# Optimization experiments

Hardware: AMD Instinct MI355X
Metric: run time of the kernel (lower is better)

## Reference

```python
import jax, jax.numpy as jnp
import numpy as np

H, W, L = 512, 512, 28
N_ITER = 12
SIGMA = 0.5
LAM = 1.0
PI = 3.141592653589793


def _offsets(s, phi_deg):
    # Matches torch: dx = s*cos(phi), dy = s*sin(phi), shifted to min 0, round-half-even.
    phi = phi_deg * PI / 180.0
    dx = s * np.cos(phi)
    dy = s * np.sin(phi)
    dx = dx - dx.min()
    dy = dy - dy.min()
    return np.rint(dx).astype(np.int32), np.rint(dy).astype(np.int32)


def _gauss_kernel(sigma):
    ksize = max(3, int(6 * sigma + 1) | 1)  # 5 for sigma=0.5
    ax = np.arange(ksize, dtype=np.float32) - ksize // 2
    g1 = np.exp(-0.5 * (ax / sigma) ** 2)
    g1 = g1 / g1.sum()
    g2 = np.outer(g1, g1).astype(np.float32)
    return jnp.asarray(g2)[None, None], ksize // 2  # [1,1,k,k], pad


def setup_inputs():
    k1, k2 = jax.random.split(jax.random.key(0))
    s_nom = jnp.arange(L, dtype=jnp.float32)
    phi_d_deg = jnp.ones((), dtype=jnp.float32)
    dx, dy = _offsets(np.arange(L, dtype=np.float32), 1.0)
    Hp, Wp = H + int(dy.max()), W + int(dx.max())
    y_1hw = jax.random.uniform(k1, (1, Hp, Wp), dtype=jnp.float32)
    mask2d = jax.random.uniform(k2, (H, W), dtype=jnp.float32)
    return {"y_1hw": y_1hw, "mask2d": mask2d, "phi_d_deg": phi_d_deg, "s_nom": s_nom}


def reference(y_1hw, mask2d, phi_d_deg, s_nom):
    # Integer dispersion offsets are detached (.item()) in the original, so they
    # are compile-time constants here.
    dx, dy = _offsets(np.asarray(s_nom), float(np.asarray(phi_d_deg)))
    Hp, Wp = H + int(dy.max()), W + int(dx.max())
    rows = dy[:, None, None] + np.arange(H, dtype=np.int64)[None, :, None]  # [L,H,1]
    cols = dx[:, None, None] + np.arange(W, dtype=np.int64)[None, None, :]  # [L,1,W]
    flat = jnp.asarray(rows * Wp + cols)  # [L,H,W] flat indices into [Hp*Wp]

    g2, pad = _gauss_kernel(SIGMA)

    def A(x):  # CASSI forward: [L,H,W] -> [Hp,Wp] batched scatter-add
        return jnp.zeros(Hp * Wp, x.dtype).at[flat].add(mask2d[None] * x).reshape(Hp, Wp)

    def At(y2):  # CASSI adjoint: [Hp,Wp] -> [L,H,W] batched gather
        return y2.reshape(-1)[flat] * mask2d[None]

    def denoise(x):  # depthwise 5x5 Gaussian; same 2D kernel per band -> bands as batch
        return jax.lax.conv_general_dilated(
            x[:, None], g2, (1, 1), [(pad, pad), (pad, pad)])[:, 0]

    # Phi_sum = sum over bands of shifted mask, clamped to >= 1
    Phi_sum = jnp.maximum(
        jnp.zeros(Hp * Wp, mask2d.dtype).at[flat].add(
            jnp.broadcast_to(mask2d[None], (L, H, W))).reshape(Hp, Wp),
        1.0)

    y = y_1hw[0]
    x = At(y)   # adjoint back-projection initialization
    y1 = y
    for _ in range(N_ITER):  # unrolled GAP iterations (accelerated GAP)
        yb = A(x)
        y1 = y1 + (y - yb)
        x = x + LAM * At((y1 - yb) / Phi_sum)
        x = denoise(x)
    return x[None]  # [1, L, H, W]
```

## Files before the change

### kernel.cpp

```cpp
#include <hip/hip_runtime.h>

#define HH 512
#define WW 512
#define LL 28
#define WP 539
#define NPIX (HH * WP)
#define NX (LL * HH * WW)

__global__ void k_setup(const float* __restrict__ y, const float* __restrict__ mask,
                        float* __restrict__ phi_inv, float* __restrict__ y1) {
    int idx = blockIdx.x * blockDim.x + threadIdx.x;
    if (idx >= NPIX) return;
    int i = idx / WP, jp = idx - i * WP;
    int lmin = jp - (WW - 1); if (lmin < 0) lmin = 0;
    int lmax = jp < (LL - 1) ? jp : (LL - 1);
    float s = 0.f;
    for (int l = lmin; l <= lmax; ++l) s += mask[i * WW + (jp - l)];
    phi_inv[idx] = 1.0f / fmaxf(s, 1.0f);
    y1[idx] = y[idx];
}

__global__ void k_xinit(const float* __restrict__ y, const float* __restrict__ mask,
                        float* __restrict__ x) {
    int idx = blockIdx.x * blockDim.x + threadIdx.x;
    if (idx >= NX) return;
    int l = idx / (HH * WW);
    int r = idx - l * HH * WW;
    int i = r / WW, j = r - i * WW;
    x[idx] = y[i * WP + j + l] * mask[i * WW + j];
}

__global__ void k_fwd(const float* __restrict__ x, const float* __restrict__ mask,
                      const float* __restrict__ y, const float* __restrict__ phi_inv,
                      float* __restrict__ y1, float* __restrict__ t) {
    int idx = blockIdx.x * blockDim.x + threadIdx.x;
    if (idx >= NPIX) return;
    int i = idx / WP, jp = idx - i * WP;
    int lmin = jp - (WW - 1); if (lmin < 0) lmin = 0;
    int lmax = jp < (LL - 1) ? jp : (LL - 1);
    float yb = 0.f;
    const float* mrow = mask + i * WW;
    for (int l = lmin; l <= lmax; ++l) {
        int j = jp - l;
        yb = fmaf(mrow[j], x[(size_t)l * HH * WW + i * WW + j], yb);
    }
    float y1n = y1[idx] + y[idx] - yb;
    y1[idx] = y1n;
    t[idx] = (y1n - yb) * phi_inv[idx];
}

#define TX 64
#define TY 16
__global__ void k_upblur(const float* __restrict__ x, const float* __restrict__ t,
                         const float* __restrict__ mask, float* __restrict__ xo,
                         float w0, float w1, float w2) {
    __shared__ float u[(TY + 4)][(TX + 4)];
    __shared__ float hb[(TY + 4)][TX];
    const int l  = blockIdx.z;
    const int bi = blockIdx.y * TY;
    const int bj = blockIdx.x * TX;
    const int tid = threadIdx.x;
    const float* xl = x + (size_t)l * HH * WW;

    for (int idx = tid; idx < (TY + 4) * (TX + 4); idx += 256) {
        int r = idx / (TX + 4), c = idx - r * (TX + 4);
        int gi = bi + r - 2, gj = bj + c - 2;
        float v = 0.f;
        if (gi >= 0 && gi < HH && gj >= 0 && gj < WW) {
            v = xl[gi * WW + gj] + t[gi * WP + gj + l] * mask[gi * WW + gj];
        }
        u[r][c] = v;
    }
    __syncthreads();

    for (int idx = tid; idx < (TY + 4) * TX; idx += 256) {
        int r = idx / TX, c = idx - r * TX;
        hb[r][c] = w2 * (u[r][c] + u[r][c + 4])
                 + w1 * (u[r][c + 1] + u[r][c + 3])
                 + w0 * u[r][c + 2];
    }
    __syncthreads();

    for (int idx = tid; idx < TY * TX; idx += 256) {
        int r = idx / TX, c = idx - r * TX;
        float o = w2 * (hb[r][c] + hb[r + 4][c])
                + w1 * (hb[r + 1][c] + hb[r + 3][c])
                + w0 * hb[r + 2][c];
        xo[((size_t)l * HH + bi + r) * WW + bj + c] = o;
    }
}

extern "C" void kernel_launch(void* const* d_in, const int* in_sizes, int n_in,
                              void* d_out, int out_size, void* d_ws, size_t ws_size,
                              hipStream_t stream) {
    const float* y    = (const float*)d_in[0];
    const float* mask = (const float*)d_in[1];

    float* out = (float*)d_out;

    float* phi_inv = (float*)d_ws;
    float* y1      = phi_inv + NPIX;
    float* t       = y1 + NPIX;
    float* xA      = t + NPIX;
    float* xB      = out;

    float g1 = expf(-2.0f), g2 = expf(-8.0f);
    float gs = 1.0f + 2.0f * g1 + 2.0f * g2;
    float w0 = 1.0f / gs, w1 = g1 / gs, w2 = g2 / gs;

    const int BT = 256;
    const int gpix = (NPIX + BT - 1) / BT;

    k_setup<<<gpix, BT, 0, stream>>>(y, mask, phi_inv, y1);
    k_xinit<<<(NX + BT - 1) / BT, BT, 0, stream>>>(y, mask, xB);

    float* cur = xB;
    float* nxt = xA;
    for (int it = 0; it < 12; ++it) {
        k_fwd<<<gpix, BT, 0, stream>>>(cur, mask, y, phi_inv, y1, t);
        k_upblur<<<dim3(WW / TX, HH / TY, LL), BT, 0, stream>>>(cur, t, mask, nxt, w0, w1, w2);
        float* tmp = cur; cur = nxt; nxt = tmp;
    }
}
```

Baseline: 460.9 us.

## Fuse forward projection into blur kernel via shared-memory partial sums and atomics

```diff
diff --git a/kernel.cpp b/kernel.cpp
--- a/kernel.cpp
+++ b/kernel.cpp
@@ -6,6 +6,11 @@
 #define WP 539
 #define NPIX (HH * WP)
 #define NX (LL * HH * WW)
+
+#define TX 64
+#define TY 16
+#define GB 7
+#define NGRP (LL / GB)
 
 __global__ void k_setup(const float* __restrict__ y, const float* __restrict__ mask,
                         float* __restrict__ phi_inv, float* __restrict__ y1) {
@@ -21,73 +26,114 @@
 }
 
 __global__ void k_xinit(const float* __restrict__ y, const float* __restrict__ mask,
-                        float* __restrict__ x) {
-    int idx = blockIdx.x * blockDim.x + threadIdx.x;
-    if (idx >= NX) return;
-    int l = idx / (HH * WW);
-    int r = idx - l * HH * WW;
-    int i = r / WW, j = r - i * WW;
-    x[idx] = y[i * WP + j + l] * mask[i * WW + j];
-}
-
-__global__ void k_fwd(const float* __restrict__ x, const float* __restrict__ mask,
-                      const float* __restrict__ y, const float* __restrict__ phi_inv,
-                      float* __restrict__ y1, float* __restrict__ t) {
-    int idx = blockIdx.x * blockDim.x + threadIdx.x;
-    if (idx >= NPIX) return;
-    int i = idx / WP, jp = idx - i * WP;
-    int lmin = jp - (WW - 1); if (lmin < 0) lmin = 0;
-    int lmax = jp < (LL - 1) ? jp : (LL - 1);
-    float yb = 0.f;
-    const float* mrow = mask + i * WW;
-    for (int l = lmin; l <= lmax; ++l) {
-        int j = jp - l;
-        yb = fmaf(mrow[j], x[(size_t)l * HH * WW + i * WW + j], yb);
-    }
-    float y1n = y1[idx] + y[idx] - yb;
-    y1[idx] = y1n;
-    t[idx] = (y1n - yb) * phi_inv[idx];
-}
-
-#define TX 64
-#define TY 16
-__global__ void k_upblur(const float* __restrict__ x, const float* __restrict__ t,
-                         const float* __restrict__ mask, float* __restrict__ xo,
-                         float w0, float w1, float w2) {
-    __shared__ float u[(TY + 4)][(TX + 4)];
-    __shared__ float hb[(TY + 4)][TX];
-    const int l  = blockIdx.z;
+                        float* __restrict__ x, float* __restrict__ yb) {
+    __shared__ float ybl[TY][TX + GB - 1];
+    const int l0 = blockIdx.z * GB;
     const int bi = blockIdx.y * TY;
     const int bj = blockIdx.x * TX;
     const int tid = threadIdx.x;
-    const float* xl = x + (size_t)l * HH * WW;
+
+    for (int idx = tid; idx < TY * (TX + GB - 1); idx += 256)
+        ybl[idx / (TX + GB - 1)][idx % (TX + GB - 1)] = 0.f;
+    __syncthreads();
+
+    for (int l = l0; l < l0 + GB; ++l) {
+        #pragma unroll
+        for (int k = 0; k < 4; ++k) {
+            int idx = tid + k * 256;
+            int r = idx / TX, c = idx - r * TX;
+            int gi = bi + r, gj = bj + c;
+            float m = mask[gi * WW + gj];
+            float v = y[gi * WP + gj + l] * m;
+            x[((size_t)l * HH + gi) * WW + gj] = v;
+            ybl[r][c + (l - l0)] += m * v;
+        }
+        __syncthreads();
+    }
+    for (int idx = tid; idx < TY * (TX + GB - 1); idx += 256) {
+        int r = idx / (TX + GB - 1), c = idx % (TX + GB - 1);
+        atomicAdd(&yb[(bi + r) * WP + bj + l0 + c], ybl[r][c]);
+    }
+}
+
+__global__ void k_pix(const float* __restrict__ y, const float* __restrict__ phi_inv,
+                      float* __restrict__ y1, float* __restrict__ t, float* __restrict__ yb) {
+    int idx = blockIdx.x * blockDim.x + threadIdx.x;
+    if (idx >= NPIX / 4) return;
+    float4 ybv = ((const float4*)yb)[idx];
+    float4 yv  = ((const float4*)y)[idx];
+    float4 y1v = ((const float4*)y1)[idx];
+    float4 pv  = ((const float4*)phi_inv)[idx];
+    float4 y1n, tv;
+    y1n.x = y1v.x + yv.x - ybv.x;  tv.x = (y1n.x - ybv.x) * pv.x;
+    y1n.y = y1v.y + yv.y - ybv.y;  tv.y = (y1n.y - ybv.y) * pv.y;
+    y1n.z = y1v.z + yv.z - ybv.z;  tv.z = (y1n.z - ybv.z) * pv.z;
+    y1n.w = y1v.w + yv.w - ybv.w;  tv.w = (y1n.w - ybv.w) * pv.w;
+    ((float4*)y1)[idx] = y1n;
+    ((float4*)t)[idx]  = tv;
+    ((float4*)yb)[idx] = make_float4(0.f, 0.f, 0.f, 0.f);
+}
+
+template <bool LAST>
+__global__ void k_iter(const float* __restrict__ x, const float* __restrict__ t,
+                       const float* __restrict__ mask, float* __restrict__ xo,
+                       float* __restrict__ yb, float w0, float w1, float w2) {
+    __shared__ float msk[TY + 4][TX + 4];
+    __shared__ float u[TY + 4][TX + 4];
+    __shared__ float hb[TY + 4][TX];
+    __shared__ float ybl[TY][TX + GB - 1];
+
+    const int l0 = blockIdx.z * GB;
+    const int bi = blockIdx.y * TY;
+    const int bj = blockIdx.x * TX;
+    const int tid = threadIdx.x;
 
     for (int idx = tid; idx < (TY + 4) * (TX + 4); idx += 256) {
         int r = idx / (TX + 4), c = idx - r * (TX + 4);
         int gi = bi + r - 2, gj = bj + c - 2;
-        float v = 0.f;
-        if (gi >= 0 && gi < HH && gj >= 0 && gj < WW) {
-            v = xl[gi * WW + gj] + t[gi * WP + gj + l] * mask[gi * WW + gj];
-        }
-        u[r][c] = v;
+        msk[r][c] = (gi >= 0 && gi < HH && gj >= 0 && gj < WW) ? mask[gi * WW + gj] : 0.f;
     }
+    if (!LAST)
+        for (int idx = tid; idx < TY * (TX + GB - 1); idx += 256)
+            ybl[idx / (TX + GB - 1)][idx % (TX + GB - 1)] = 0.f;
     __syncthreads();
 
-    for (int idx = tid; idx < (TY + 4) * TX; idx += 256) {
-        int r = idx / TX, c = idx - r * TX;
-        hb[r][c] = w2 * (u[r][c] + u[r][c + 4])
-                 + w1 * (u[r][c + 1] + u[r][c + 3])
-                 + w0 * u[r][c + 2];
+    for (int l = l0; l < l0 + GB; ++l) {
+        const float* xl = x + (size_t)l * HH * WW;
+        for (int idx = tid; idx < (TY + 4) * (TX + 4); idx += 256) {
+            int r = idx / (TX + 4), c = idx - r * (TX + 4);
+            int gi = bi + r - 2, gj = bj + c - 2;
+            float v = 0.f;
+            if (gi >= 0 && gi < HH && gj >= 0 && gj < WW)
+                v = xl[gi * WW + gj] + t[gi * WP + gj + l] * msk[r][c];
+            u[r][c] = v;
+        }
+        __syncthreads();
+        for (int idx = tid; idx < (TY + 4) * TX; idx += 256) {
+            int r = idx / TX, c = idx - r * TX;
+            hb[r][c] = w2 * (u[r][c] + u[r][c + 4])
+                     + w1 * (u[r][c + 1] + u[r][c + 3])
+                     + w0 * u[r][c + 2];
+        }
+        __syncthreads();
+        #pragma unroll
+        for (int k = 0; k < 4; ++k) {
+            int idx = tid + k * 256;
+            int r = idx / TX, c = idx - r * TX;
+            float o = w2 * (hb[r][c] + hb[r + 4][c])
+                    + w1 * (hb[r + 1][c] + hb[r + 3][c])
+                    + w0 * hb[r + 2][c];
+            xo[((size_t)l * HH + bi + r) * WW + bj + c] = o;
+            if (!LAST) ybl[r][c + (l - l0)] += msk[r + 2][c + 2] * o;
+        }
+        __syncthreads();
     }
-    __syncthreads();
 
-    for (int idx = tid; idx < TY * TX; idx += 256) {
-        int r = idx / TX, c = idx - r * TX;
-        float o = w2 * (hb[r][c] + hb[r + 4][c])
-                + w1 * (hb[r + 1][c] + hb[r + 3][c])
-                + w0 * hb[r + 2][c];
-        xo[((size_t)l * HH + bi + r) * WW + bj + c] = o;
-    }
+    if (!LAST)
+        for (int idx = tid; idx < TY * (TX + GB - 1); idx += 256) {
+            int r = idx / (TX + GB - 1), c = idx % (TX + GB - 1);
+            atomicAdd(&yb[(bi + r) * WP + bj + l0 + c], ybl[r][c]);
+        }
 }
 
 extern "C" void kernel_launch(void* const* d_in, const int* in_sizes, int n_in,
@@ -101,7 +147,8 @@
     float* phi_inv = (float*)d_ws;
     float* y1      = phi_inv + NPIX;
     float* t       = y1 + NPIX;
-    float* xA      = t + NPIX;
+    float* yb      = t + NPIX;
+    float* xA      = yb + NPIX;
     float* xB      = out;
 
     float g1 = expf(-2.0f), g2 = expf(-8.0f);
@@ -109,16 +156,20 @@
     float w0 = 1.0f / gs, w1 = g1 / gs, w2 = g2 / gs;
 
     const int BT = 256;
-    const int gpix = (NPIX + BT - 1) / BT;
+    const dim3 tgrid(WW / TX, HH / TY, NGRP);
 
-    k_setup<<<gpix, BT, 0, stream>>>(y, mask, phi_inv, y1);
-    k_xinit<<<(NX + BT - 1) / BT, BT, 0, stream>>>(y, mask, xB);
+    hipMemsetAsync(yb, 0, NPIX * sizeof(float), stream);
+    k_setup<<<(NPIX + BT - 1) / BT, BT, 0, stream>>>(y, mask, phi_inv, y1);
+    k_xinit<<<tgrid, BT, 0, stream>>>(y, mask, xB, yb);
 
     float* cur = xB;
     float* nxt = xA;
     for (int it = 0; it < 12; ++it) {
-        k_fwd<<<gpix, BT, 0, stream>>>(cur, mask, y, phi_inv, y1, t);
-        k_upblur<<<dim3(WW / TX, HH / TY, LL), BT, 0, stream>>>(cur, t, mask, nxt, w0, w1, w2);
+        k_pix<<<(NPIX / 4 + BT - 1) / BT, BT, 0, stream>>>(y, phi_inv, y1, t, yb);
+        if (it < 11)
+            k_iter<false><<<tgrid, BT, 0, stream>>>(cur, t, mask, nxt, yb, w0, w1, w2);
+        else
+            k_iter<true><<<tgrid, BT, 0, stream>>>(cur, t, mask, nxt, yb, w0, w1, w2);
         float* tmp = cur; cur = nxt; nxt = tmp;
     }
 }
```

Result: slower. 484.1 us (+5.0%).

## Fuse forward projection into blur via atomics and store bands in half precision

Applied to the files above, without the earlier changes.

```diff
diff --git a/kernel.cpp b/kernel.cpp
--- a/kernel.cpp
+++ b/kernel.cpp
@@ -1,4 +1,5 @@
 #include <hip/hip_runtime.h>
+#include <hip/hip_fp16.h>
 
 #define HH 512
 #define WW 512
@@ -7,86 +8,129 @@
 #define NPIX (HH * WP)
 #define NX (LL * HH * WW)
 
-__global__ void k_setup(const float* __restrict__ y, const float* __restrict__ mask,
-                        float* __restrict__ phi_inv, float* __restrict__ y1) {
+#define TX 64
+#define TY 16
+
+__global__ __launch_bounds__(256) void k_setup(const float* __restrict__ y,
+                                               const float* __restrict__ mask,
+                                               float* __restrict__ phi_inv,
+                                               float* __restrict__ y1,
+                                               float* __restrict__ yb) {
     int idx = blockIdx.x * blockDim.x + threadIdx.x;
     if (idx >= NPIX) return;
     int i = idx / WP, jp = idx - i * WP;
     int lmin = jp - (WW - 1); if (lmin < 0) lmin = 0;
     int lmax = jp < (LL - 1) ? jp : (LL - 1);
-    float s = 0.f;
-    for (int l = lmin; l <= lmax; ++l) s += mask[i * WW + (jp - l)];
+    float s = 0.f, sq = 0.f;
+    const float* mrow = mask + i * WW;
+    for (int l = lmin; l <= lmax; ++l) {
+        float m = mrow[jp - l];
+        s += m; sq = fmaf(m, m, sq);
+    }
     phi_inv[idx] = 1.0f / fmaxf(s, 1.0f);
-    y1[idx] = y[idx];
+    float yv = y[idx];
+    y1[idx] = yv;
+    yb[idx] = yv * sq;
 }
 
-__global__ void k_xinit(const float* __restrict__ y, const float* __restrict__ mask,
-                        float* __restrict__ x) {
+__global__ __launch_bounds__(256) void k_xinit(const float* __restrict__ y,
+                                               const float* __restrict__ mask,
+                                               __half* __restrict__ x) {
     int idx = blockIdx.x * blockDim.x + threadIdx.x;
-    if (idx >= NX) return;
-    int l = idx / (HH * WW);
-    int r = idx - l * HH * WW;
-    int i = r / WW, j = r - i * WW;
-    x[idx] = y[i * WP + j + l] * mask[i * WW + j];
+    if (idx >= NX / 2) return;
+    int p = idx * 2;
+    int l = p / (HH * WW);
+    int r = p - l * HH * WW;
+    int i = r >> 9, j = r & 511;
+    const float* yrow = y + i * WP + l;
+    const float* mrow = mask + i * WW;
+    __half2 v = __floats2half2_rn(yrow[j] * mrow[j], yrow[j + 1] * mrow[j + 1]);
+    *reinterpret_cast<__half2*>(x + p) = v;
 }
 
-__global__ void k_fwd(const float* __restrict__ x, const float* __restrict__ mask,
-                      const float* __restrict__ y, const float* __restrict__ phi_inv,
-                      float* __restrict__ y1, float* __restrict__ t) {
+__global__ __launch_bounds__(256) void k_pix(const float* __restrict__ y,
+                                             const float* __restrict__ phi_inv,
+                                             float* __restrict__ y1,
+                                             float* __restrict__ t,
+                                             float* __restrict__ yb) {
     int idx = blockIdx.x * blockDim.x + threadIdx.x;
-    if (idx >= NPIX) return;
-    int i = idx / WP, jp = idx - i * WP;
-    int lmin = jp - (WW - 1); if (lmin < 0) lmin = 0;
-    int lmax = jp < (LL - 1) ? jp : (LL - 1);
-    float yb = 0.f;
-    const float* mrow = mask + i * WW;
-    for (int l = lmin; l <= lmax; ++l) {
-        int j = jp - l;
-        yb = fmaf(mrow[j], x[(size_t)l * HH * WW + i * WW + j], yb);
-    }
-    float y1n = y1[idx] + y[idx] - yb;
-    y1[idx] = y1n;
-    t[idx] = (y1n - yb) * phi_inv[idx];
+    if (idx >= NPIX / 4) return;
+    float4 ybv = ((const float4*)yb)[idx];
+    float4 yv  = ((const float4*)y)[idx];
+    float4 y1v = ((const float4*)y1)[idx];
+    float4 pv  = ((const float4*)phi_inv)[idx];
+    float4 y1n, tv;
+    y1n.x = y1v.x + yv.x - ybv.x;  tv.x = (y1n.x - ybv.x) * pv.x;
+    y1n.y = y1v.y + yv.y - ybv.y;  tv.y = (y1n.y - ybv.y) * pv.y;
+    y1n.z = y1v.z + yv.z - ybv.z;  tv.z = (y1n.z - ybv.z) * pv.z;
+    y1n.w = y1v.w + yv.w - ybv.w;  tv.w = (y1n.w - ybv.w) * pv.w;
+    ((float4*)y1)[idx] = y1n;
+    ((float4*)t)[idx]  = tv;
+    ((float4*)yb)[idx] = make_float4(0.f, 0.f, 0.f, 0.f);
 }
 
-#define TX 64
-#define TY 16
-__global__ void k_upblur(const float* __restrict__ x, const float* __restrict__ t,
-                         const float* __restrict__ mask, float* __restrict__ xo,
-                         float w0, float w1, float w2) {
-    __shared__ float u[(TY + 4)][(TX + 4)];
-    __shared__ float hb[(TY + 4)][TX];
+template <bool LAST>
+__global__ __launch_bounds__(256) void k_band(const __half* __restrict__ xin,
+                                              const float* __restrict__ t,
+                                              const float* __restrict__ mask,
+                                              void* __restrict__ xout,
+                                              float* __restrict__ yb,
+                                              float w0, float w1, float w2) {
+    __shared__ float u[TY + 4][TX + 4];
+    __shared__ float hb[TY + 4][TX];
+
     const int l  = blockIdx.z;
     const int bi = blockIdx.y * TY;
     const int bj = blockIdx.x * TX;
     const int tid = threadIdx.x;
-    const float* xl = x + (size_t)l * HH * WW;
+    const int tx = tid & 63;
+    const int ty = tid >> 6;
+    const __half* xl = xin + (size_t)l * HH * WW;
 
-    for (int idx = tid; idx < (TY + 4) * (TX + 4); idx += 256) {
-        int r = idx / (TX + 4), c = idx - r * (TX + 4);
-        int gi = bi + r - 2, gj = bj + c - 2;
-        float v = 0.f;
-        if (gi >= 0 && gi < HH && gj >= 0 && gj < WW) {
-            v = xl[gi * WW + gj] + t[gi * WP + gj + l] * mask[gi * WW + gj];
+    #pragma unroll
+    for (int k = 0; k < 5; ++k) {
+        int r = ty + 4 * k;
+        int gi = bi + r - 2;
+        bool rok = (gi >= 0) & (gi < HH);
+        int gj0 = bj + tx - 2;
+        float v0 = 0.f;
+        if (rok & (gj0 >= 0) & (gj0 < WW))
+            v0 = fmaf(t[gi * WP + gj0 + l], mask[gi * WW + gj0],
+                      __half2float(xl[gi * WW + gj0]));
+        u[r][tx] = v0;
+        if (tx < 4) {
+            int gj1 = bj + 64 + tx - 2;
+            float v1 = 0.f;
+            if (rok & (gj1 < WW))
+                v1 = fmaf(t[gi * WP + gj1 + l], mask[gi * WW + gj1],
+                          __half2float(xl[gi * WW + gj1]));
+            u[r][64 + tx] = v1;
         }
-        u[r][c] = v;
     }
     __syncthreads();
 
-    for (int idx = tid; idx < (TY + 4) * TX; idx += 256) {
-        int r = idx / TX, c = idx - r * TX;
-        hb[r][c] = w2 * (u[r][c] + u[r][c + 4])
-                 + w1 * (u[r][c + 1] + u[r][c + 3])
-                 + w0 * u[r][c + 2];
+    #pragma unroll
+    for (int k = 0; k < 5; ++k) {
+        int r = ty + 4 * k;
+        hb[r][tx] = w2 * (u[r][tx] + u[r][tx + 4])
+                  + w1 * (u[r][tx + 1] + u[r][tx + 3])
+                  + w0 * u[r][tx + 2];
     }
     __syncthreads();
 
-    for (int idx = tid; idx < TY * TX; idx += 256) {
-        int r = idx / TX, c = idx - r * TX;
-        float o = w2 * (hb[r][c] + hb[r + 4][c])
-                + w1 * (hb[r + 1][c] + hb[r + 3][c])
-                + w0 * hb[r + 2][c];
-        xo[((size_t)l * HH + bi + r) * WW + bj + c] = o;
+    #pragma unroll
+    for (int k = 0; k < 4; ++k) {
+        int r = ty + 4 * k;
+        float o = w2 * (hb[r][tx] + hb[r + 4][tx])
+                + w1 * (hb[r + 1][tx] + hb[r + 3][tx])
+                + w0 * hb[r + 2][tx];
+        int gi = bi + r, gj = bj + tx;
+        if (LAST) {
+            ((float*)xout)[((size_t)l * HH + gi) * WW + gj] = o;
+        } else {
+            ((__half*)xout)[((size_t)l * HH + gi) * WW + gj] = __float2half(o);
+            atomicAdd(&yb[gi * WP + gj + l], mask[gi * WW + gj] * o);
+        }
     }
 }
 
@@ -95,30 +139,33 @@
                               hipStream_t stream) {
     const float* y    = (const float*)d_in[0];
     const float* mask = (const float*)d_in[1];
-
     float* out = (float*)d_out;
 
     float* phi_inv = (float*)d_ws;
     float* y1      = phi_inv + NPIX;
     float* t       = y1 + NPIX;
-    float* xA      = t + NPIX;
-    float* xB      = out;
+    float* yb      = t + NPIX;
+    __half* xA     = (__half*)(yb + NPIX);
+    __half* xB     = xA + NX;
 
     float g1 = expf(-2.0f), g2 = expf(-8.0f);
     float gs = 1.0f + 2.0f * g1 + 2.0f * g2;
     float w0 = 1.0f / gs, w1 = g1 / gs, w2 = g2 / gs;
 
-    const int BT = 256;
-    const int gpix = (NPIX + BT - 1) / BT;
+    const dim3 bgrid(WW / TX, HH / TY, LL);
 
-    k_setup<<<gpix, BT, 0, stream>>>(y, mask, phi_inv, y1);
-    k_xinit<<<(NX + BT - 1) / BT, BT, 0, stream>>>(y, mask, xB);
+    k_setup<<<(NPIX + 255) / 256, 256, 0, stream>>>(y, mask, phi_inv, y1, yb);
+    k_xinit<<<(NX / 2 + 255) / 256, 256, 0, stream>>>(y, mask, xA);
 
-    float* cur = xB;
-    float* nxt = xA;
+    __half* cur = xA;
+    __half* nxt = xB;
     for (int it = 0; it < 12; ++it) {
-        k_fwd<<<gpix, BT, 0, stream>>>(cur, mask, y, phi_inv, y1, t);
-        k_upblur<<<dim3(WW / TX, HH / TY, LL), BT, 0, stream>>>(cur, t, mask, nxt, w0, w1, w2);
-        float* tmp = cur; cur = nxt; nxt = tmp;
+        k_pix<<<(NPIX / 4 + 255) / 256, 256, 0, stream>>>(y, phi_inv, y1, t, yb);
+        if (it < 11) {
+            k_band<false><<<bgrid, 256, 0, stream>>>(cur, t, mask, (void*)nxt, yb, w0, w1, w2);
+            __half* tmp = cur; cur = nxt; nxt = tmp;
+        } else {
+            k_band<true><<<bgrid, 256, 0, stream>>>(cur, t, mask, (void*)out, yb, w0, w1, w2);
+        }
     }
 }
```

New measurement: 581.7 us. 1.26x slower.
